# Performance work log

Hardware: AMD Instinct MI355X
Metric: run time of the kernel (lower is better)

## Reference

```python
import jax, jax.numpy as jnp
import numpy as np

N, E, G = 50000, 800000, 500
D, H, L, C, P = 256, 128, 2, 2, 128


def gcn(h, W, b, src, dst, ew, n):
    # PyG GCNConv: x@W, add self-loops (weight 1), sym-normalized aggregation at dst, + bias
    x = h @ W
    deg = jnp.ones((n,), x.dtype).at[dst].add(ew)  # self-loop contributes 1
    dinv = jax.lax.rsqrt(deg)
    norm = dinv[src] * ew * dinv[dst]
    out = jax.ops.segment_sum(x[src] * norm[:, None], dst, num_segments=n)
    out = out + x * (dinv * dinv)[:, None]  # self-loop message
    return out + b


def setup_inputs() -> dict:
    key = jax.random.key(0)
    ks = iter(jax.random.split(key, 64))

    def p(shape, s=0.05):
        return jax.random.normal(next(ks), shape, jnp.float32) * s

    inp = {
        'x': jax.random.normal(next(ks), (N, D), jnp.float32),
        'edge_index': jax.random.randint(next(ks), (2, E), 0, N),
        'edge_weight': jax.random.uniform(next(ks), (E,), jnp.float32),
        'batch': jnp.sort(jax.random.randint(next(ks), (N,), 0, G)),
        'eeg_mask': jax.random.randint(next(ks), (N,), 0, 2).astype(jnp.int32),
        'num_graphs': G,
        'eeg_W': p((D, H)), 'eeg_b': jnp.zeros((H,), jnp.float32),
        'fnirs_W': p((D, H)), 'fnirs_b': jnp.zeros((H,), jnp.float32),
        'edge_W1': p((H + 1, 64)), 'edge_b1': jnp.zeros((64,), jnp.float32),
        'edge_W2': p((64, 1)), 'edge_b2': jnp.zeros((1,), jnp.float32),
        'conv_intra_W': p((L, H, H)), 'conv_intra_b': jnp.zeros((L, H), jnp.float32),
        'conv_cross_W': p((L, H, H)), 'conv_cross_b': jnp.zeros((L, H), jnp.float32),
        'rel_gate': jnp.zeros((L,), jnp.float32),
        'bn_gamma': jnp.ones((L, H), jnp.float32), 'bn_beta': jnp.zeros((L, H), jnp.float32),
        'co_W1': p((3 * H, H)), 'co_b1': jnp.zeros((H,), jnp.float32),
        'co_W2': p((H, 2)), 'co_b2': jnp.zeros((2,), jnp.float32),
        'gate_W1': p((2 * H, H)), 'gate_b1': jnp.zeros((H,), jnp.float32),
        'gate_W2': p((H, 1)), 'gate_b2': jnp.zeros((1,), jnp.float32),
        'cls_W1': p((H, H // 2)), 'cls_b1': jnp.zeros((H // 2,), jnp.float32),
        'cls_W2': p((H // 2, C)), 'cls_b2': jnp.zeros((C,), jnp.float32),
        'pe_W1': p((H, H)), 'pe_b1': jnp.zeros((H,), jnp.float32),
        'pe_W2': p((H, P)), 'pe_b2': jnp.zeros((P,), jnp.float32),
        'pf_W1': p((H, H)), 'pf_b1': jnp.zeros((H,), jnp.float32),
        'pf_W2': p((H, P)), 'pf_b2': jnp.zeros((P,), jnp.float32),
    }
    return inp


def reference(x, edge_index, edge_weight, batch, eeg_mask, num_graphs,
              eeg_W, eeg_b, fnirs_W, fnirs_b,
              edge_W1, edge_b1, edge_W2, edge_b2,
              conv_intra_W, conv_intra_b, conv_cross_W, conv_cross_b,
              rel_gate, bn_gamma, bn_beta,
              co_W1, co_b1, co_W2, co_b2,
              gate_W1, gate_b1, gate_W2, gate_b2,
              cls_W1, cls_b1, cls_W2, cls_b2,
              pe_W1, pe_b1, pe_W2, pe_b2,
              pf_W1, pf_b1, pf_W2, pf_b2):
    n = x.shape[0]
    src, dst = edge_index[0], edge_index[1]
    em = eeg_mask.astype(bool)
    emf = em.astype(x.dtype)
    # modality-aware projection (select per node)
    h = jnp.where(em[:, None], jax.nn.relu(x @ eeg_W + eeg_b), jax.nn.relu(x @ fnirs_W + fnirs_b))
    # edge modulation: MLP on (|h_src - h_dst|, w)
    diff = jnp.abs(h[src] - h[dst])  # [E, H]
    eh = jax.nn.relu(jnp.concatenate([diff, edge_weight[:, None]], axis=1) @ edge_W1 + edge_b1)
    g = jax.nn.sigmoid((eh @ edge_W2 + edge_b2)[:, 0])
    ew_hat = edge_weight * jnp.clip(g, 0.2, 1.2)
    # intra/cross relation split via weight masking (same math as edge subsetting)
    intra = (em[src] == em[dst]).astype(x.dtype)
    ew_intra = ew_hat * intra
    ew_cross = ew_hat * (1.0 - intra)
    for l in range(conv_intra_W.shape[0]):
        hi = gcn(h, conv_intra_W[l], conv_intra_b[l], src, dst, ew_intra, n)
        hc = gcn(h, conv_cross_W[l], conv_cross_b[l], src, dst, ew_cross, n)
        h = hi + jax.nn.sigmoid(rel_gate[l]) * hc
        mu = h.mean(0)
        var = h.var(0)  # biased, as in torch BN training
        h = bn_gamma[l] * (h - mu) * jax.lax.rsqrt(var + 1e-5) + bn_beta[l]
        h = jax.nn.relu(h)  # dropout: eval mode (identity)

    def pool(w):
        s = jax.ops.segment_sum(h * w[:, None], batch, num_segments=num_graphs)
        c = jax.ops.segment_sum(w, batch, num_segments=num_graphs)
        return s / jnp.maximum(c, 1.0)[:, None]

    h_global = pool(jnp.ones((n,), x.dtype))
    h_e = pool(emf)
    h_f = pool(1.0 - emf)
    co = jnp.concatenate([h_e, h_f, h_e * h_f], axis=-1)
    alpha = jax.nn.sigmoid(jax.nn.relu(co @ co_W1 + co_b1) @ co_W2 + co_b2)
    alpha = alpha / (alpha.sum(-1, keepdims=True) + 1e-6)
    h_cr = alpha[:, :1] * h_e + alpha[:, 1:] * h_f
    gte = jax.nn.sigmoid(jax.nn.relu(jnp.concatenate([h_cr, h_global], -1) @ gate_W1 + gate_b1) @ gate_W2 + gate_b2)
    h_final = gte * h_cr + (1.0 - gte) * h_global
    logits = jax.nn.relu(h_final @ cls_W1 + cls_b1) @ cls_W2 + cls_b2

    def l2n(z):
        return z / jnp.maximum(jnp.linalg.norm(z, axis=-1, keepdims=True), 1e-12)

    z_e = l2n(jax.nn.relu(h_e @ pe_W1 + pe_b1) @ pe_W2 + pe_b2)
    z_f = l2n(jax.nn.relu(h_f @ pf_W1 + pf_b1) @ pf_W2 + pf_b2)
    return logits, z_e, z_f
```

## Files before the change

### kernel.cpp

```cpp
#include <hip/hip_runtime.h>
#include <math.h>

#define H 128
#define D 256

typedef __attribute__((ext_vector_type(8))) short bf16x8;
typedef __attribute__((ext_vector_type(4))) float f32x4;

__device__ __forceinline__ float sigmoidf_(float x){ return 1.0f/(1.0f+__expf(-x)); }

__device__ __forceinline__ unsigned int bfr_(float f){
  unsigned int u = __float_as_uint(f);
  return (u + 0x7fffu + ((u>>16)&1u)) >> 16;
}

__device__ __forceinline__ void split2(float a, float b, unsigned &hi, unsigned &lo){
  unsigned ha = bfr_(a), hb2 = bfr_(b);
  float fa = __uint_as_float(ha<<16), fb = __uint_as_float(hb2<<16);
  unsigned la = bfr_(a - fa), lb = bfr_(b - fb);
  hi = ha | (hb2<<16); lo = la | (lb<<16);
}

__device__ __forceinline__ unsigned pair_dft(unsigned a, unsigned b){
  float a0 = __uint_as_float(a<<16), a1 = __uint_as_float(a & 0xffff0000u);
  float b0 = __uint_as_float(b<<16), b1 = __uint_as_float(b & 0xffff0000u);
  unsigned d0 = __float_as_uint(fabsf(a0-b0));
  unsigned d1 = __float_as_uint(fabsf(a1-b1));
  return __builtin_amdgcn_perm(d1, d0, 0x07060302);
}

__global__ void k_prepall(const float* __restrict__ eegW, const float* __restrict__ fnW,
                          const float* __restrict__ cIW, const float* __restrict__ cCW,
                          const float* __restrict__ eW1,
                          unsigned short* WeF, unsigned short* WfF,
                          unsigned short* WIf0, unsigned short* WCf0,
                          unsigned short* WIf1, unsigned short* WCf1,
                          unsigned short* W1b)
{
  int b = blockIdx.x;
  int t = threadIdx.x;
  if (b < 64){
    const float* W; unsigned short* out; int ksteps; int boff;
    if (b < 16){ W=eegW; out=WeF; ksteps=8; boff=b; }
    else if (b < 32){ W=fnW; out=WfF; ksteps=8; boff=b-16; }
    else if (b < 40){ W=cIW;        out=WIf0; ksteps=4; boff=b-32; }
    else if (b < 48){ W=cCW;        out=WCf0; ksteps=4; boff=b-40; }
    else if (b < 56){ W=cIW+16384;  out=WIf1; ksteps=4; boff=b-48; }
    else            { W=cCW+16384;  out=WCf1; ksteps=4; boff=b-56; }
    int id = boff*256 + t;
    if (id >= ksteps*8*64) return;
    int lane = id & 63;
    int mfrag = (id>>6) & 7;
    int kstep = id >> 9;
    int col = mfrag*16 + (lane&15);
    int k0 = kstep*32 + (lane>>4)*8;
    unsigned short* oh = out + (size_t)(((kstep*8+mfrag)*2+0)*64 + lane)*8;
    unsigned short* ol = out + (size_t)(((kstep*8+mfrag)*2+1)*64 + lane)*8;
    #pragma unroll
    for (int j=0;j<8;j++){
      float w = W[(size_t)(k0+j)*128 + col];
      unsigned h16 = bfr_(w);
      float hf = __uint_as_float(h16<<16);
      oh[j] = (unsigned short)h16;
      ol[j] = (unsigned short)bfr_(w - hf);
    }
  } else {
    for (int it=0; it<4; it++){
      int le = it*256 + t;
      int f = le >> 6, lane = le & 63;
      int kstep = f >> 2, n = f & 3;
      int col = n*16 + (lane & 15);
      int k0 = kstep*32 + ((lane>>4)&3)*8;
      unsigned short* op = W1b + (size_t)le*8;
      #pragma unroll
      for (int j=0;j<8;j++)
        op[j] = (unsigned short)bfr_(eW1[(size_t)(k0+j)*64 + col]);
    }
  }
}

__global__ __launch_bounds__(256) void k_projm(
    const float* __restrict__ x, const int* __restrict__ em,
    const unsigned short* __restrict__ WeF, const float* __restrict__ be,
    const unsigned short* __restrict__ WfF, const float* __restrict__ bf,
    float* __restrict__ h, unsigned int* __restrict__ hb, int N)
{
  int t = threadIdx.x;
  int lane = t & 63;
  int base = (blockIdx.x*4 + (t>>6))*16;
  if (base >= N) return;
  int node = base + (lane & 15);
  int nodeL = min(node, N-1);
  int ko = lane >> 4;

  f32x4 accE[8], accF[8];
  #pragma unroll
  for (int mf=0;mf<8;mf++){ accE[mf]=(f32x4){0.f,0.f,0.f,0.f}; accF[mf]=(f32x4){0.f,0.f,0.f,0.f}; }

  const bf16x8* we = reinterpret_cast<const bf16x8*>(WeF);
  const bf16x8* wf = reinterpret_cast<const bf16x8*>(WfF);

  for (int kstep=0;kstep<8;kstep++){
    const float4* xr = reinterpret_cast<const float4*>(x + (size_t)nodeL*D + kstep*32 + ko*8);
    float4 v0 = xr[0], v1 = xr[1];
    uint4 hiu, lou;
    split2(v0.x, v0.y, hiu.x, lou.x);
    split2(v0.z, v0.w, hiu.y, lou.y);
    split2(v1.x, v1.y, hiu.z, lou.z);
    split2(v1.z, v1.w, hiu.w, lou.w);
    bf16x8 Bhi = *reinterpret_cast<bf16x8*>(&hiu);
    bf16x8 Blo = *reinterpret_cast<bf16x8*>(&lou);
    #pragma unroll
    for (int mf=0;mf<8;mf++){
      int fb = (kstep*8+mf)*2;
      bf16x8 aEh = we[(size_t)fb*64 + lane];
      bf16x8 aEl = we[(size_t)(fb+1)*64 + lane];
      accE[mf] = __builtin_amdgcn_mfma_f32_16x16x32_bf16(aEh, Bhi, accE[mf], 0,0,0);
      accE[mf] = __builtin_amdgcn_mfma_f32_16x16x32_bf16(aEh, Blo, accE[mf], 0,0,0);
      accE[mf] = __builtin_amdgcn_mfma_f32_16x16x32_bf16(aEl, Bhi, accE[mf], 0,0,0);
      bf16x8 aFh = wf[(size_t)fb*64 + lane];
      bf16x8 aFl = wf[(size_t)(fb+1)*64 + lane];
      accF[mf] = __builtin_amdgcn_mfma_f32_16x16x32_bf16(aFh, Bhi, accF[mf], 0,0,0);
      accF[mf] = __builtin_amdgcn_mfma_f32_16x16x32_bf16(aFh, Blo, accF[mf], 0,0,0);
      accF[mf] = __builtin_amdgcn_mfma_f32_16x16x32_bf16(aFl, Bhi, accF[mf], 0,0,0);
    }
  }
  if (node >= N) return;
  bool e = em[node] != 0;
  #pragma unroll
  for (int mf=0;mf<8;mf++){
    float sv[4];
    #pragma unroll
    for (int r=0;r<4;r++){
      int ch = mf*16 + ko*4 + r;
      float vE = accE[mf][r] + be[ch];
      float vF = accF[mf][r] + bf[ch];
      sv[r] = fmaxf(e ? vE : vF, 0.f);
    }
    float2* hp = reinterpret_cast<float2*>(h + (size_t)node*H + mf*16 + ko*4);
    hp[0] = make_float2(sv[0], sv[1]);
    hp[1] = make_float2(sv[2], sv[3]);
    unsigned int* hbp = hb + (size_t)node*64 + mf*8 + ko*2;
    hbp[0] = bfr_(sv[0]) | (bfr_(sv[1])<<16);
    hbp[1] = bfr_(sv[2]) | (bfr_(sv[3])<<16);
  }
}

__global__ __launch_bounds__(256) void k_gemm2m(
    const float* __restrict__ A,
    const unsigned short* __restrict__ WIf, const unsigned short* __restrict__ WCf,
    const float* __restrict__ bna, const float* __restrict__ bnb2,
    unsigned int* __restrict__ tIb, unsigned int* __restrict__ tCb, int N)
{
  int t = threadIdx.x;
  int lane = t & 63;
  int base = (blockIdx.x*4 + (t>>6))*16;
  if (base >= N) return;
  int node = base + (lane & 15);
  int nodeL = min(node, N-1);
  int ko = lane >> 4;

  f32x4 accI[8], accC[8];
  #pragma unroll
  for (int mf=0;mf<8;mf++){ accI[mf]=(f32x4){0.f,0.f,0.f,0.f}; accC[mf]=(f32x4){0.f,0.f,0.f,0.f}; }

  const bf16x8* wi = reinterpret_cast<const bf16x8*>(WIf);
  const bf16x8* wc = reinterpret_cast<const bf16x8*>(WCf);
  bool doBN = (bna != nullptr);

  for (int kstep=0;kstep<4;kstep++){
    const float4* ar = reinterpret_cast<const float4*>(A + (size_t)nodeL*H + kstep*32 + ko*8);
    float4 v0 = ar[0], v1 = ar[1];
    if (doBN){
      int ch = kstep*32 + ko*8;
      const float4* a4 = reinterpret_cast<const float4*>(bna + ch);
      const float4* b4 = reinterpret_cast<const float4*>(bnb2 + ch);
      float4 a0 = a4[0], a1 = a4[1], bb0 = b4[0], bb1 = b4[1];
      v0.x = fmaxf(fmaf(a0.x, v0.x, bb0.x), 0.f);
      v0.y = fmaxf(fmaf(a0.y, v0.y, bb0.y), 0.f);
      v0.z = fmaxf(fmaf(a0.z, v0.z, bb0.z), 0.f);
      v0.w = fmaxf(fmaf(a0.w, v0.w, bb0.w), 0.f);
      v1.x = fmaxf(fmaf(a1.x, v1.x, bb1.x), 0.f);
      v1.y = fmaxf(fmaf(a1.y, v1.y, bb1.y), 0.f);
      v1.z = fmaxf(fmaf(a1.z, v1.z, bb1.z), 0.f);
      v1.w = fmaxf(fmaf(a1.w, v1.w, bb1.w), 0.f);
    }
    uint4 hiu, lou;
    split2(v0.x, v0.y, hiu.x, lou.x);
    split2(v0.z, v0.w, hiu.y, lou.y);
    split2(v1.x, v1.y, hiu.z, lou.z);
    split2(v1.z, v1.w, hiu.w, lou.w);
    bf16x8 Bhi = *reinterpret_cast<bf16x8*>(&hiu);
    bf16x8 Blo = *reinterpret_cast<bf16x8*>(&lou);
    #pragma unroll
    for (int mf=0;mf<8;mf++){
      int fb = (kstep*8+mf)*2;
      bf16x8 aIh = wi[(size_t)fb*64 + lane];
      bf16x8 aIl = wi[(size_t)(fb+1)*64 + lane];
      accI[mf] = __builtin_amdgcn_mfma_f32_16x16x32_bf16(aIh, Bhi, accI[mf], 0,0,0);
      accI[mf] = __builtin_amdgcn_mfma_f32_16x16x32_bf16(aIh, Blo, accI[mf], 0,0,0);
      accI[mf] = __builtin_amdgcn_mfma_f32_16x16x32_bf16(aIl, Bhi, accI[mf], 0,0,0);
      bf16x8 aCh = wc[(size_t)fb*64 + lane];
      bf16x8 aCl = wc[(size_t)(fb+1)*64 + lane];
      accC[mf] = __builtin_amdgcn_mfma_f32_16x16x32_bf16(aCh, Bhi, accC[mf], 0,0,0);
      accC[mf] = __builtin_amdgcn_mfma_f32_16x16x32_bf16(aCh, Blo, accC[mf], 0,0,0);
      accC[mf] = __builtin_amdgcn_mfma_f32_16x16x32_bf16(aCl, Bhi, accC[mf], 0,0,0);
    }
  }
  if (node >= N) return;
  #pragma unroll
  for (int mf=0;mf<8;mf++){
    unsigned int* ti = tIb + (size_t)node*64 + mf*8 + ko*2;
    unsigned int* tc = tCb + (size_t)node*64 + mf*8 + ko*2;
    ti[0] = bfr_(accI[mf][0]) | (bfr_(accI[mf][1])<<16);
    ti[1] = bfr_(accI[mf][2]) | (bfr_(accI[mf][3])<<16);
    tc[0] = bfr_(accC[mf][0]) | (bfr_(accC[mf][1])<<16);
    tc[1] = bfr_(accC[mf][2]) | (bfr_(accC[mf][3])<<16);
  }
}

__global__ void k_hist(const int* __restrict__ ei, int* __restrict__ cnt, int E){
  int e = blockIdx.x*blockDim.x + threadIdx.x;
  if (e < E) atomicAdd(cnt + ei[E+e], 1);
}

__global__ __launch_bounds__(1024) void k_scan(const int* __restrict__ cnt,
                                               int* __restrict__ start, int N){
  __shared__ int sm[1024];
  int t = threadIdx.x;
  int chunk = (N + 1023)/1024;
  int i0 = t*chunk, i1 = min(i0+chunk, N);
  int s = 0;
  for (int i=i0;i<i1;i++) s += cnt[i];
  sm[t] = s; __syncthreads();
  for (int d=1; d<1024; d<<=1){
    int v = (t>=d)? sm[t-d] : 0;
    __syncthreads();
    sm[t] += v;
    __syncthreads();
  }
  int base = (t==0)? 0 : sm[t-1];
  for (int i=i0;i<i1;i++){ start[i] = base; base += cnt[i]; }
  if (t == 1023) start[N] = base;
}

__global__ void k_fill2(const int* __restrict__ ei, const int* __restrict__ em,
                        const float* __restrict__ ew,
                        const int* __restrict__ start, int* __restrict__ wcnt,
                        int* __restrict__ csr_sc, int* __restrict__ csr_d,
                        float* __restrict__ csr_w, int E){
  int e = blockIdx.x*blockDim.x + threadIdx.x;
  if (e >= E) return;
  int s = ei[e], d = ei[E+e];
  int chan = (em[s] == em[d]) ? 0 : 1;
  int pos = start[d] + atomicAdd(wcnt + d, 1);
  csr_sc[pos] = (s<<1) | chan;
  csr_d[pos] = d;
  csr_w[pos] = ew[e];
}

__global__ __launch_bounds__(256) void k_edgem(
    const unsigned int* __restrict__ hb,
    const int* __restrict__ csr_sc, const int* __restrict__ csr_d,
    const float* __restrict__ csr_w, const unsigned short* __restrict__ W1b,
    const float* __restrict__ W1, const float* __restrict__ b1,
    const float* __restrict__ W2, const float* __restrict__ b2,
    float* __restrict__ csr_cf,
    float* __restrict__ degI, float* __restrict__ degC, int E)
{
  __shared__ uint4 wlds[1024];
  int t = threadIdx.x;
  {
    const uint4* src = reinterpret_cast<const uint4*>(W1b);
    #pragma unroll
    for (int i=0;i<4;i++) wlds[i*256 + t] = src[i*256 + t];
  }
  __syncthreads();

  int lane = t & 63;
  int base0 = (blockIdx.x*4 + (t>>6)) * 32;
  if (base0 >= E) return;

  int colbase = lane & 15;
  int ko = lane >> 4;
  float w1l[4], b1v[4], w2v[4];
  #pragma unroll
  for (int n=0;n<4;n++){
    int col = n*16 + colbase;
    w1l[n] = W1[(size_t)128*64 + col];
    b1v[n] = b1[col];
    w2v[n] = W2[col];
  }
  float bb2 = b2[0];

  uint4 us[2][4], ud[2][4];
  #pragma unroll
  for (int eg=0; eg<2; eg++){
    int e = min(base0 + eg*16 + colbase, E-1);
    int s = csr_sc[e] >> 1;
    int d = csr_d[e];
    const uint4* hsp = reinterpret_cast<const uint4*>(hb + (size_t)s*64);
    const uint4* hdp = reinterpret_cast<const uint4*>(hb + (size_t)d*64);
    #pragma unroll
    for (int kstep=0;kstep<4;kstep++){
      us[eg][kstep] = hsp[kstep*4 + ko];
      ud[eg][kstep] = hdp[kstep*4 + ko];
    }
  }

  const bf16x8* wl = reinterpret_cast<const bf16x8*>(wlds);
  #pragma unroll
  for (int eg=0; eg<2; eg++){
    int base = base0 + eg*16;
    if (base >= E) break;

    f32x4 acc[4];
    #pragma unroll
    for (int n=0;n<4;n++) acc[n] = (f32x4){0.f,0.f,0.f,0.f};

    #pragma unroll
    for (int kstep=0;kstep<4;kstep++){
      uint4 pa;
      pa.x = pair_dft(us[eg][kstep].x, ud[eg][kstep].x);
      pa.y = pair_dft(us[eg][kstep].y, ud[eg][kstep].y);
      pa.z = pair_dft(us[eg][kstep].z, ud[eg][kstep].z);
      pa.w = pair_dft(us[eg][kstep].w, ud[eg][kstep].w);
      bf16x8 a = *reinterpret_cast<bf16x8*>(&pa);
      #pragma unroll
      for (int n=0;n<4;n++)
        acc[n] = __builtin_amdgcn_mfma_f32_16x16x32_bf16(a, wl[(kstep*4+n)*64 + lane], acc[n], 0,0,0);
    }

    float wgtr[4];
    #pragma unroll
    for (int r=0;r<4;r++)
      wgtr[r] = csr_w[min(base + ko*4 + r, E-1)];

    float part[4] = {0.f,0.f,0.f,0.f};
    #pragma unroll
    for (int n=0;n<4;n++){
      #pragma unroll
      for (int r=0;r<4;r++){
        float v = fmaxf(acc[n][r] + fmaf(wgtr[r], w1l[n], b1v[n]), 0.f);
        part[r] = fmaf(v, w2v[n], part[r]);
      }
    }
    #pragma unroll
    for (int m=1;m<16;m<<=1){
      #pragma unroll
      for (int r=0;r<4;r++) part[r] += __shfl_xor(part[r], m, 64);
    }

    if (colbase == 0){
      #pragma unroll
      for (int r=0;r<4;r++){
        int ee = base + ko*4 + r;
        if (ee < E){
          float g = sigmoidf_(part[r] + bb2);
          g = fminf(fmaxf(g, 0.2f), 1.2f);
          float ehat = wgtr[r] * g;
          csr_cf[ee] = ehat;
          int sc2 = csr_sc[ee];
          atomicAdd(((sc2&1) ? degC : degI) + csr_d[ee], ehat);
        }
      }
    }
  }
}

__global__ void k_dinv(const float* __restrict__ degI, const float* __restrict__ degC,
                       float* dinvI, float* dinvC, int N){
  int i = blockIdx.x*blockDim.x + threadIdx.x;
  if (i < N){
    dinvI[i] = rsqrtf(1.f + degI[i]);
    dinvC[i] = rsqrtf(1.f + degC[i]);
  }
}

__global__ void k_scale(const int* __restrict__ csr_sc, const int* __restrict__ csr_d,
                        const float* __restrict__ dinvI, const float* __restrict__ dinvC,
                        float* __restrict__ csr_cf, int E){
  int k = blockIdx.x*blockDim.x + threadIdx.x;
  if (k >= E) return;
  int sc = csr_sc[k];
  int s = sc>>1;
  int d = csr_d[k];
  const float* dv = (sc&1) ? dinvC : dinvI;
  csr_cf[k] *= dv[s]*dv[d];
}

__global__ void k_bnab(const float* __restrict__ bnsum, const float* __restrict__ bnsq,
                       const float* __restrict__ gamma, const float* __restrict__ beta,
                       float invN, float* __restrict__ bna, float* __restrict__ bnb2){
  int j = threadIdx.x;
  float mu = bnsum[j]*invN;
  float var = bnsq[j]*invN - mu*mu;
  float r = rsqrtf(var + 1e-5f);
  float a = gamma[j]*r;
  bna[j] = a;
  bnb2[j] = beta[j] - a*mu;
}

__global__ __launch_bounds__(256) void k_aggrb(
    const unsigned int* __restrict__ tIb, const unsigned int* __restrict__ tCb,
    const int* __restrict__ start, const int* __restrict__ csr_sc,
    const float* __restrict__ csr_cf,
    const float* __restrict__ dinvI, const float* __restrict__ dinvC,
    const float* __restrict__ bI, const float* __restrict__ bC,
    const float* __restrict__ relg, int l,
    float* __restrict__ h, int N)
{
  int lane = threadIdx.x & 63;
  int d = blockIdx.x*4 + (threadIdx.x>>6);
  if (d >= N) return;
  float sig = sigmoidf_(relg[l]);
  int k0 = start[d], k1 = start[d+1];
  float ax=0.f, ay=0.f;
  int k = k0;
  for (; k+8 <= k1; k += 8){
    unsigned vv[8]; float cc[8];
    #pragma unroll
    for (int u=0;u<8;u++){
      int sc = csr_sc[k+u];
      float cf = csr_cf[k+u];
      vv[u] = ((sc&1) ? tCb : tIb)[(size_t)(sc>>1)*64 + lane];
      cc[u] = (sc&1) ? sig*cf : cf;
    }
    #pragma unroll
    for (int u=0;u<8;u++){
      ax = fmaf(cc[u], __uint_as_float(vv[u]<<16), ax);
      ay = fmaf(cc[u], __uint_as_float(vv[u] & 0xffff0000u), ay);
    }
  }
  for (; k < k1; ++k){
    int sc = csr_sc[k];
    float cf = csr_cf[k];
    unsigned v = ((sc&1) ? tCb : tIb)[(size_t)(sc>>1)*64 + lane];
    float ce = (sc&1) ? sig*cf : cf;
    ax = fmaf(ce, __uint_as_float(v<<16), ax);
    ay = fmaf(ce, __uint_as_float(v & 0xffff0000u), ay);
  }
  float diI = dinvI[d], diC = dinvC[d];
  float rI = diI*diI, rC = diC*diC;
  unsigned vi = tIb[(size_t)d*64 + lane];
  unsigned vc = tCb[(size_t)d*64 + lane];
  int off = lane*2;
  float ox = fmaf(__uint_as_float(vi<<16), rI, bI[off])
           + sig*fmaf(__uint_as_float(vc<<16), rC, bC[off]) + ax;
  float oy = fmaf(__uint_as_float(vi & 0xffff0000u), rI, bI[off+1])
           + sig*fmaf(__uint_as_float(vc & 0xffff0000u), rC, bC[off+1]) + ay;
  *reinterpret_cast<float2*>(h + (size_t)d*H + off) = make_float2(ox, oy);
}

__global__ __launch_bounds__(128) void k_stats(const float* __restrict__ h,
    float* __restrict__ bnsum, float* __restrict__ bnsq, int N, int nper)
{
  int j = threadIdx.x;
  int n0 = blockIdx.x*nper, n1 = min(n0+nper, N);
  if (n0 >= N) return;
  float sl=0.f, sq=0.f;
  for (int n=n0;n<n1;n++){
    float v = h[(size_t)n*H+j];
    sl += v; sq = fmaf(v,v,sq);
  }
  atomicAdd(bnsum+j, sl); atomicAdd(bnsq+j, sq);
}

__global__ __launch_bounds__(128) void k_poolbn(
    const float* __restrict__ h, const int* __restrict__ batch, const int* __restrict__ em,
    const float* __restrict__ bnsum, const float* __restrict__ bnsq,
    const float* __restrict__ gamma, const float* __restrict__ beta, float invN,
    float* __restrict__ sumE, float* __restrict__ sumF,
    float* __restrict__ cntE, float* __restrict__ cntF, int N, int nper)
{
  int j = threadIdx.x;
  int n0 = blockIdx.x*nper, n1 = min(n0+nper, N);
  if (n0 >= N) return;
  float mu = bnsum[j]*invN;
  float var = bnsq[j]*invN - mu*mu;
  float rr = rsqrtf(var + 1e-5f);
  float ga = gamma[j], be = beta[j];
  float aE=0.f, aF=0.f, ce=0.f, cfc=0.f;
  int cg = batch[n0];
  for (int n=n0;n<n1;n++){
    int g = batch[n];
    if (g != cg){
      atomicAdd(sumE+(size_t)cg*H+j, aE);
      atomicAdd(sumF+(size_t)cg*H+j, aF);
      if (j==0){ atomicAdd(cntE+cg, ce); atomicAdd(cntF+cg, cfc); }
      aE=aF=ce=cfc=0.f; cg=g;
    }
    float v = fmaxf(fmaf(ga, (h[(size_t)n*H+j]-mu)*rr, be), 0.f);
    bool eb = em[n] != 0;
    if (eb) aE += v; else aF += v;
    if (j==0){ if (eb) ce += 1.f; else cfc += 1.f; }
  }
  atomicAdd(sumE+(size_t)cg*H+j, aE);
  atomicAdd(sumF+(size_t)cg*H+j, aF);
  if (j==0){ atomicAdd(cntE+cg, ce); atomicAdd(cntF+cg, cfc); }
}

__device__ __forceinline__ float blockReduceSum(float v, float* red){
  int t = threadIdx.x;
  red[t] = v; __syncthreads();
  #pragma unroll
  for (int s=64;s>0;s>>=1){ if (t<s) red[t]+=red[t+s]; __syncthreads(); }
  float r = red[0]; __syncthreads();
  return r;
}

__global__ __launch_bounds__(128) void k_head(
    const float* __restrict__ sumE, const float* __restrict__ sumF,
    const float* __restrict__ cntE, const float* __restrict__ cntF,
    const float* __restrict__ coW1, const float* __restrict__ cob1,
    const float* __restrict__ coW2, const float* __restrict__ cob2,
    const float* __restrict__ gW1, const float* __restrict__ gb1,
    const float* __restrict__ gW2, const float* __restrict__ gb2,
    const float* __restrict__ cW1, const float* __restrict__ cb1,
    const float* __restrict__ cW2, const float* __restrict__ cb2,
    const float* __restrict__ peW1, const float* __restrict__ peb1,
    const float* __restrict__ peW2, const float* __restrict__ peb2,
    const float* __restrict__ pfW1, const float* __restrict__ pfb1,
    const float* __restrict__ pfW2, const float* __restrict__ pfb2,
    float* __restrict__ out, int G)
{
  int g = blockIdx.x, j = threadIdx.x;
  __shared__ float sh[384];
  __shared__ float red[128];
  __shared__ float hfin[128], buf[128];
  float cE = cntE[g], cF = cntF[g];
  float se = sumE[(size_t)g*H+j], sf = sumF[(size_t)g*H+j];
  float he = se/fmaxf(cE,1.f), hf = sf/fmaxf(cF,1.f);
  float hg = (se+sf)/fmaxf(cE+cF,1.f);
  sh[j]=he; sh[128+j]=hf; sh[256+j]=he*hf;
  __syncthreads();
  float a = cob1[j];
  for (int k=0;k<384;k++) a = fmaf(sh[k], coW1[k*H+j], a);
  a = fmaxf(a, 0.f);
  float r0 = blockReduceSum(a*coW2[2*j],   red);
  float r1 = blockReduceSum(a*coW2[2*j+1], red);
  float al0 = sigmoidf_(r0 + cob2[0]);
  float al1 = sigmoidf_(r1 + cob2[1]);
  float asum = al0+al1+1e-6f; al0/=asum; al1/=asum;
  float hc = al0*he + al1*hf;
  __syncthreads();
  sh[j]=hc; sh[128+j]=hg;
  __syncthreads();
  float gg = gb1[j];
  for (int k=0;k<256;k++) gg = fmaf(sh[k], gW1[k*H+j], gg);
  gg = fmaxf(gg, 0.f);
  float gt = sigmoidf_(blockReduceSum(gg*gW2[j], red) + gb2[0]);
  float hfj = gt*hc + (1.f-gt)*hg;
  hfin[j] = hfj;
  __syncthreads();
  float c1v = 0.f;
  if (j < 64){
    float c1 = cb1[j];
    for (int k=0;k<128;k++) c1 = fmaf(hfin[k], cW1[k*64+j], c1);
    c1v = fmaxf(c1, 0.f);
  }
  float l0 = blockReduceSum(j<64 ? c1v*cW2[2*j]   : 0.f, red);
  float l1 = blockReduceSum(j<64 ? c1v*cW2[2*j+1] : 0.f, red);
  if (j==0){ out[(size_t)g*2] = l0 + cb2[0]; out[(size_t)g*2+1] = l1 + cb2[1]; }
  buf[j] = he; __syncthreads();
  float q = peb1[j];
  for (int k=0;k<128;k++) q = fmaf(buf[k], peW1[k*H+j], q);
  q = fmaxf(q, 0.f);
  __syncthreads(); sh[j] = q; __syncthreads();
  float z = peb2[j];
  for (int k=0;k<128;k++) z = fmaf(sh[k], peW2[k*H+j], z);
  float nr = sqrtf(blockReduceSum(z*z, red));
  out[(size_t)G*2 + (size_t)g*H + j] = z / fmaxf(nr, 1e-12f);
  __syncthreads(); buf[j] = hf; __syncthreads();
  float q2 = pfb1[j];
  for (int k=0;k<128;k++) q2 = fmaf(buf[k], pfW1[k*H+j], q2);
  q2 = fmaxf(q2, 0.f);
  __syncthreads(); sh[j] = q2; __syncthreads();
  float z2 = pfb2[j];
  for (int k=0;k<128;k++) z2 = fmaf(sh[k], pfW2[k*H+j], z2);
  float nr2 = sqrtf(blockReduceSum(z2*z2, red));
  out[(size_t)G*2 + (size_t)G*H + (size_t)g*H + j] = z2 / fmaxf(nr2, 1e-12f);
}

extern "C" void kernel_launch(void* const* d_in, const int* in_sizes, int n_in,
                              void* d_out, int out_size, void* d_ws, size_t ws_size,
                              hipStream_t stream)
{
  const float* x    = (const float*)d_in[0];
  const int*   ei   = (const int*)d_in[1];
  const float* ew   = (const float*)d_in[2];
  const int*   batch= (const int*)d_in[3];
  const int*   em   = (const int*)d_in[4];
  const float* eegW = (const float*)d_in[6];  const float* eegB = (const float*)d_in[7];
  const float* fnW  = (const float*)d_in[8];  const float* fnB  = (const float*)d_in[9];
  const float* eW1  = (const float*)d_in[10]; const float* eb1  = (const float*)d_in[11];
  const float* eW2  = (const float*)d_in[12]; const float* eb2  = (const float*)d_in[13];
  const float* cIW  = (const float*)d_in[14]; const float* cIb  = (const float*)d_in[15];
  const float* cCW  = (const float*)d_in[16]; const float* cCb  = (const float*)d_in[17];
  const float* relg = (const float*)d_in[18];
  const float* bng  = (const float*)d_in[19]; const float* bnb  = (const float*)d_in[20];
  const float* coW1 = (const float*)d_in[21]; const float* cob1 = (const float*)d_in[22];
  const float* coW2 = (const float*)d_in[23]; const float* cob2 = (const float*)d_in[24];
  const float* gW1  = (const float*)d_in[25]; const float* gb1  = (const float*)d_in[26];
  const float* gW2  = (const float*)d_in[27]; const float* gb2  = (const float*)d_in[28];
  const float* cW1  = (const float*)d_in[29]; const float* cb1  = (const float*)d_in[30];
  const float* cW2  = (const float*)d_in[31]; const float* cb2  = (const float*)d_in[32];
  const float* peW1 = (const float*)d_in[33]; const float* peb1 = (const float*)d_in[34];
  const float* peW2 = (const float*)d_in[35]; const float* peb2 = (const float*)d_in[36];
  const float* pfW1 = (const float*)d_in[37]; const float* pfb1 = (const float*)d_in[38];
  const float* pfW2 = (const float*)d_in[39]; const float* pfb2 = (const float*)d_in[40];
  float* out = (float*)d_out;

  int N = in_sizes[0] / D;
  int E = in_sizes[2];
  int G = out_size / (2 + 2*H);
  int NH = N*H;

  float* p = (float*)d_ws;
  float* h    = p; p += (size_t)NH;
  float* tI   = p; p += (size_t)NH;
  float* tC   = p; p += (size_t)NH;
  float* csr_cf = p; p += E;
  float* csr_w  = p; p += E;
  int* csr_sc = (int*)p; p += E;
  int* csr_d  = (int*)p; p += E;
  int* start  = (int*)p; p += (N+1);
  int* cnt    = (int*)p; p += N;
  int* wcnt   = (int*)p; p += N;
  float* degI = p; p += N;
  float* degC = p; p += N;
  float* dinvI= p; p += N;
  float* dinvC= p; p += N;
  float* bnsum= p; p += H;
  float* bnsq = p; p += H;
  float* bna  = p; p += H;
  float* bnb2 = p; p += H;
  float* sumE = p; p += (size_t)G*H;
  float* sumF = p; p += (size_t)G*H;
  float* cntE = p; p += G;
  float* cntF = p; p += G;
  unsigned short* W1b = (unsigned short*)p; p += 4096;
  unsigned short* WeF = (unsigned short*)p; p += 32768;
  unsigned short* WfF = (unsigned short*)p; p += 32768;
  unsigned short* WIf0= (unsigned short*)p; p += 16384;
  unsigned short* WCf0= (unsigned short*)p; p += 16384;
  unsigned short* WIf1= (unsigned short*)p; p += 16384;
  unsigned short* WCf1= (unsigned short*)p; p += 16384;

  unsigned int* hb  = (unsigned int*)tI;
  unsigned int* tIb = (unsigned int*)tI;
  unsigned int* tCb = (unsigned int*)tC;

  int mmBlocks = ((N+15)/16 + 3)/4;
  int edgeBlocks = (E + 127)/128;
  int statBlocks = 1024;
  int nper_stat = (N + statBlocks - 1)/statBlocks;
  int poolBlocks = (N + 31)/32;

  hipMemsetAsync(cnt, 0, (size_t)4*N*sizeof(int), stream);
  k_hist<<<(E+255)/256,256,0,stream>>>(ei, cnt, E);
  k_scan<<<1,1024,0,stream>>>(cnt, start, N);
  k_fill2<<<(E+255)/256,256,0,stream>>>(ei, em, ew, start, wcnt,
                                        csr_sc, csr_d, csr_w, E);
  k_prepall<<<65,256,0,stream>>>(eegW, fnW, cIW, cCW, eW1,
                                 WeF, WfF, WIf0, WCf0, WIf1, WCf1, W1b);

  k_projm<<<mmBlocks,256,0,stream>>>(x, em, WeF, eegB, WfF, fnB, h, hb, N);
  k_edgem<<<edgeBlocks,256,0,stream>>>(hb, csr_sc, csr_d, csr_w, W1b,
                                       eW1, eb1, eW2, eb2, csr_cf, degI, degC, E);
  k_dinv<<<(N+255)/256,256,0,stream>>>(degI,degC,dinvI,dinvC,N);
  k_scale<<<(E+255)/256,256,0,stream>>>(csr_sc, csr_d, dinvI, dinvC, csr_cf, E);

  k_gemm2m<<<mmBlocks,256,0,stream>>>(h, WIf0, WCf0, nullptr, nullptr, tIb, tCb, N);
  k_aggrb<<<(N+3)/4,256,0,stream>>>(tIb, tCb, start, csr_sc, csr_cf,
                                    dinvI, dinvC, cIb, cCb, relg, 0, h, N);
  hipMemsetAsync(bnsum, 0, 2*H*sizeof(float), stream);
  k_stats<<<statBlocks,128,0,stream>>>(h, bnsum, bnsq, N, nper_stat);
  k_bnab<<<1,128,0,stream>>>(bnsum, bnsq, bng, bnb, 1.0f/(float)N, bna, bnb2);

  k_gemm2m<<<mmBlocks,256,0,stream>>>(h, WIf1, WCf1, bna, bnb2, tIb, tCb, N);
  k_aggrb<<<(N+3)/4,256,0,stream>>>(tIb, tCb, start, csr_sc, csr_cf,
                                    dinvI, dinvC, cIb+(size_t)H, cCb+(size_t)H,
                                    relg, 1, h, N);
  hipMemsetAsync(bnsum, 0, 2*H*sizeof(float), stream);
  k_stats<<<statBlocks,128,0,stream>>>(h, bnsum, bnsq, N, nper_stat);

  hipMemsetAsync(sumE, 0, ((size_t)2*G*H + 2*G)*sizeof(float), stream);
  k_poolbn<<<poolBlocks,128,0,stream>>>(h, batch, em, bnsum, bnsq,
                                        bng+(size_t)H, bnb+(size_t)H, 1.0f/(float)N,
                                        sumE, sumF, cntE, cntF, N, 32);
  k_head<<<G,128,0,stream>>>(sumE,sumF,cntE,cntF,
                             coW1,cob1,coW2,cob2, gW1,gb1,gW2,gb2,
                             cW1,cb1,cW2,cb2, peW1,peb1,peW2,peb2,
                             pfW1,pfb1,pfW2,pfb2, out, G);
}
```

Baseline: 651.6 us.

## Parallelize CSR offset scan across blocks and prefetch projection inputs

Replaces the single-block serial-chunk prefix scan over node counts with a two-kernel multi-block scan. Each block does a wavefront-shuffle scan, and a second pass adds the preceding block totals. It also software-prefetches the next k-step of x in the projection GEMM and unrolls the k loops in both GEMM kernels. This targets the latency of the one-block scan and the load stalls in the matmuls, at the cost of an extra launch and more registers. bsum is sized for 64 blocks, enough for the N used here.

Result: faster. 597.5 us (-8.3%).

```diff
diff --git a/kernel.cpp b/kernel.cpp
--- a/kernel.cpp
+++ b/kernel.cpp
@@ -99,10 +99,16 @@
 
   const bf16x8* we = reinterpret_cast<const bf16x8*>(WeF);
   const bf16x8* wf = reinterpret_cast<const bf16x8*>(WfF);
-
+  const float4* xr0 = reinterpret_cast<const float4*>(x + (size_t)nodeL*D + ko*8);
+
+  float4 nv0 = xr0[0], nv1 = xr0[1];
+  #pragma unroll
   for (int kstep=0;kstep<8;kstep++){
-    const float4* xr = reinterpret_cast<const float4*>(x + (size_t)nodeL*D + kstep*32 + ko*8);
-    float4 v0 = xr[0], v1 = xr[1];
+    float4 v0 = nv0, v1 = nv1;
+    if (kstep < 7){
+      nv0 = xr0[(kstep+1)*8];
+      nv1 = xr0[(kstep+1)*8 + 1];
+    }
     uint4 hiu, lou;
     split2(v0.x, v0.y, hiu.x, lou.x);
     split2(v0.z, v0.w, hiu.y, lou.y);
@@ -168,6 +174,7 @@
   const bf16x8* wc = reinterpret_cast<const bf16x8*>(WCf);
   bool doBN = (bna != nullptr);
 
+  #pragma unroll
   for (int kstep=0;kstep<4;kstep++){
     const float4* ar = reinterpret_cast<const float4*>(A + (size_t)nodeL*H + kstep*32 + ko*8);
     float4 v0 = ar[0], v1 = ar[1];
@@ -224,24 +231,46 @@
   if (e < E) atomicAdd(cnt + ei[E+e], 1);
 }
 
-__global__ __launch_bounds__(1024) void k_scan(const int* __restrict__ cnt,
-                                               int* __restrict__ start, int N){
-  __shared__ int sm[1024];
+__global__ __launch_bounds__(1024) void k_scanA(const int* __restrict__ cnt,
+                                                int* __restrict__ start,
+                                                int* __restrict__ bsum, int N){
+  __shared__ int wsum[16];
   int t = threadIdx.x;
-  int chunk = (N + 1023)/1024;
-  int i0 = t*chunk, i1 = min(i0+chunk, N);
-  int s = 0;
-  for (int i=i0;i<i1;i++) s += cnt[i];
-  sm[t] = s; __syncthreads();
-  for (int d=1; d<1024; d<<=1){
-    int v = (t>=d)? sm[t-d] : 0;
-    __syncthreads();
-    sm[t] += v;
-    __syncthreads();
-  }
-  int base = (t==0)? 0 : sm[t-1];
-  for (int i=i0;i<i1;i++){ start[i] = base; base += cnt[i]; }
-  if (t == 1023) start[N] = base;
+  int lane = t & 63, wid = t >> 6;
+  int i = blockIdx.x*1024 + t;
+  int v = (i < N) ? cnt[i] : 0;
+  int s = v;
+  #pragma unroll
+  for (int d=1; d<64; d<<=1){
+    int u = __shfl_up(s, d, 64);
+    if (lane >= d) s += u;
+  }
+  if (lane == 63) wsum[wid] = s;
+  __syncthreads();
+  if (wid == 0){
+    int w = (lane < 16) ? wsum[lane] : 0;
+    #pragma unroll
+    for (int d=1; d<16; d<<=1){
+      int u = __shfl_up(w, d, 64);
+      if (lane >= d) w += u;
+    }
+    if (lane < 16) wsum[lane] = w;
+  }
+  __syncthreads();
+  int incl = s + ((wid > 0) ? wsum[wid-1] : 0);
+  if (i < N) start[i] = incl - v;
+  if (t == 1023) bsum[blockIdx.x] = incl;
+}
+
+__global__ __launch_bounds__(1024) void k_scanC(int* __restrict__ start,
+                                                const int* __restrict__ bsum,
+                                                int N, int nb){
+  int b = blockIdx.x, t = threadIdx.x;
+  int o = 0;
+  for (int j=0;j<b;j++) o += bsum[j];
+  int i = b*1024 + t;
+  if (i < N) start[i] += o;
+  if (b == nb-1 && t == 0) start[N] = o + bsum[b];
 }
 
 __global__ void k_fill2(const int* __restrict__ ei, const int* __restrict__ em,
@@ -639,6 +668,7 @@
   float* sumF = p; p += (size_t)G*H;
   float* cntE = p; p += G;
   float* cntF = p; p += G;
+  int* bsum   = (int*)p; p += 64;
   unsigned short* W1b = (unsigned short*)p; p += 4096;
   unsigned short* WeF = (unsigned short*)p; p += 32768;
   unsigned short* WfF = (unsigned short*)p; p += 32768;
@@ -656,10 +686,12 @@
   int statBlocks = 1024;
   int nper_stat = (N + statBlocks - 1)/statBlocks;
   int poolBlocks = (N + 31)/32;
+  int scanBlocks = (N + 1023)/1024;
 
   hipMemsetAsync(cnt, 0, (size_t)4*N*sizeof(int), stream);
   k_hist<<<(E+255)/256,256,0,stream>>>(ei, cnt, E);
-  k_scan<<<1,1024,0,stream>>>(cnt, start, N);
+  k_scanA<<<scanBlocks,1024,0,stream>>>(cnt, start, bsum, N);
+  k_scanC<<<scanBlocks,1024,0,stream>>>(start, bsum, N, scanBlocks);
   k_fill2<<<(E+255)/256,256,0,stream>>>(ei, em, ew, start, wcnt,
                                         csr_sc, csr_d, csr_w, E);
   k_prepall<<<65,256,0,stream>>>(eegW, fnW, cIW, cCW, eW1,
```
